# Optimization experiments

Measured on AMD Instinct MI355X. Metric: run time of the kernel, lower is better.

The kernel has to match this reference:

```python
import jax, jax.numpy as jnp
import numpy as np

D = 2048
NUM_HEADS = 16
HEAD_DIM = D // NUM_HEADS
B, T = 4, 2048
NEG = -1e9


def setup_inputs() -> dict:
    key = jax.random.key(0)
    ks = jax.random.split(key, 6)
    X = jax.random.normal(ks[0], (B, T, D), dtype=jnp.float32)
    # additive causal mask, broadcast over batch and heads
    causal = jnp.tril(jnp.ones((T, T), dtype=jnp.float32))
    mask = jnp.where(causal == 1, 0.0, NEG)[None, None, :, :]
    scale = np.sqrt(2.0 / D).astype(np.float32)
    wq_w = jax.random.normal(ks[1], (D, D), dtype=jnp.float32) * scale
    wk_w = jax.random.normal(ks[2], (D, D), dtype=jnp.float32) * scale
    wv_w = jax.random.normal(ks[3], (D, D), dtype=jnp.float32) * scale
    wo_w = jax.random.normal(ks[4], (D, D), dtype=jnp.float32) * scale
    zeros = jnp.zeros((D,), dtype=jnp.float32)
    return {
        "X": X, "mask": mask,
        "wq_w": wq_w, "wq_b": zeros,
        "wk_w": wk_w, "wk_b": zeros,
        "wv_w": wv_w, "wv_b": zeros,
        "wo_w": wo_w, "wo_b": zeros,
    }


def reference(X, mask, wq_w, wq_b, wk_w, wk_b, wv_w, wv_b, wo_w, wo_b):
    b, t, d = X.shape
    # project and split heads: [b, h, t, hd]
    def proj(w, bias):
        return (X @ w + bias).reshape(b, t, NUM_HEADS, HEAD_DIM).transpose(0, 2, 1, 3)
    Q = proj(wq_w, wq_b)
    K = proj(wk_w, wk_b)
    V = proj(wv_w, wv_b)
    scores = jnp.einsum("bhqd,bhkd->bhqk", Q, K) / np.sqrt(HEAD_DIM).astype(X.dtype)
    scores = scores + mask
    A = jax.nn.softmax(scores, axis=-1)
    ctx = jnp.einsum("bhqk,bhkd->bhqd", A, V)  # [b, h, t, hd]
    ctx = ctx.transpose(0, 2, 1, 3).reshape(b, t, d)
    return ctx @ wo_w + wo_b
```

## Files before the change

kernel.cpp:

```cpp
#include <hip/hip_runtime.h>
#include <stdint.h>

#define DMODEL 2048
#define NH 16
#define HD 128
#define BATCH 4
#define SEQ 2048
#define MTOT (BATCH * SEQ)
#define LOG2E 1.44269504088896340736f

typedef __bf16 bf16x8 __attribute__((ext_vector_type(8)));
typedef float floatx4 __attribute__((ext_vector_type(4)));

__device__ __forceinline__ uint16_t f2b(float f) {
    union { float f; uint32_t i; } v; v.f = f;
    uint32_t r = v.i + 0x7fffu + ((v.i >> 16) & 1u);
    return (uint16_t)(r >> 16);
}

__global__ __launch_bounds__(256) void cvt_bf16(const float* __restrict__ in,
                                                uint16_t* __restrict__ out, int n) {
    const int i = (blockIdx.x * 256 + threadIdx.x) * 8;
    if (i >= n) return;
    const float4 a = *(const float4*)(in + i);
    const float4 b = *(const float4*)(in + i + 4);
    uint16_t v[8] __attribute__((aligned(16))) = {
        f2b(a.x), f2b(a.y), f2b(a.z), f2b(a.w),
        f2b(b.x), f2b(b.y), f2b(b.z), f2b(b.w)};
    *(uint4*)(out + i) = *(const uint4*)v;
}

__global__ __launch_bounds__(256) void tr_wf(const float* __restrict__ in,
                                             uint16_t* __restrict__ out) {
    __shared__ float t[64 * 69];
    const int tid = threadIdx.x;
    const int r0 = blockIdx.y * 64, c0 = blockIdx.x * 64;
    const int rr = tid >> 2, c16 = (tid & 3) << 4;
#pragma unroll
    for (int j = 0; j < 4; j++)
        *(float4*)&t[rr * 69 + c16 + j * 4] =
            *(const float4*)(in + (size_t)(r0 + rr) * DMODEL + c0 + c16 + j * 4);
    __syncthreads();
    const int oc = tid >> 2, r16 = (tid & 3) << 4;
    uint16_t v[16] __attribute__((aligned(16)));
#pragma unroll
    for (int j = 0; j < 16; j++) v[j] = f2b(t[(r16 + j) * 69 + oc]);
    uint16_t* o = out + (size_t)(c0 + oc) * DMODEL + r0 + r16;
    *(uint4*)o = *(const uint4*)v;
    *(uint4*)(o + 8) = *(const uint4*)(v + 8);
}

__global__ __launch_bounds__(256, 2) void gemm(const uint16_t* __restrict__ A,
                                               const uint16_t* __restrict__ Bt,
                                               const float* __restrict__ bias,
                                               void* __restrict__ Cout,
                                               float scale, int out_f32) {
    __shared__ __attribute__((aligned(16))) uint16_t As[128 * 32];
    __shared__ __attribute__((aligned(16))) uint16_t Bs[128 * 32];
    const int tid = threadIdx.x, lane = tid & 63, w = tid >> 6;
    const int wr = w >> 1, wc = w & 1;
    const int col = lane & 15, quad = lane >> 4;
    const long m0 = (long)blockIdx.y * 128, n0 = (long)blockIdx.x * 128;

    floatx4 acc[4][4];
#pragma unroll
    for (int i = 0; i < 4; i++)
#pragma unroll
        for (int j = 0; j < 4; j++) acc[i][j] = (floatx4){0.f, 0.f, 0.f, 0.f};

    const int srow = tid >> 2, sc = (tid & 3) << 3;
    const uint16_t* Ag0 = A + (m0 + srow) * DMODEL + sc;
    const uint16_t* Bg0 = Bt + (n0 + srow) * DMODEL + sc;
    const long rstep = (long)64 * DMODEL;

    for (int kt = 0; kt < DMODEL; kt += 32) {
        const uint4 a0 = *(const uint4*)(Ag0 + kt);
        const uint4 a1 = *(const uint4*)(Ag0 + rstep + kt);
        const uint4 b0 = *(const uint4*)(Bg0 + kt);
        const uint4 b1 = *(const uint4*)(Bg0 + rstep + kt);
        *(uint4*)&As[tid * 8] = a0;
        *(uint4*)&As[2048 + tid * 8] = a1;
        *(uint4*)&Bs[tid * 8] = b0;
        *(uint4*)&Bs[2048 + tid * 8] = b1;
        __syncthreads();
        bf16x8 af[4], bfr[4];
#pragma unroll
        for (int i = 0; i < 4; i++)
            af[i] = *(const bf16x8*)&As[(wr * 64 + i * 16 + col) * 32 + quad * 8];
#pragma unroll
        for (int j = 0; j < 4; j++)
            bfr[j] = *(const bf16x8*)&Bs[(wc * 64 + j * 16 + col) * 32 + quad * 8];
#pragma unroll
        for (int i = 0; i < 4; i++)
#pragma unroll
            for (int j = 0; j < 4; j++)
                acc[i][j] = __builtin_amdgcn_mfma_f32_16x16x32_bf16(af[i], bfr[j],
                                                                    acc[i][j], 0, 0, 0);
        __syncthreads();
    }

    float bv[4];
#pragma unroll
    for (int j = 0; j < 4; j++) bv[j] = bias[n0 + wc * 64 + j * 16 + col];
#pragma unroll
    for (int i = 0; i < 4; i++) {
        const long row = m0 + wr * 64 + i * 16 + quad * 4;
#pragma unroll
        for (int j = 0; j < 4; j++) {
            const long cc = n0 + wc * 64 + j * 16 + col;
#pragma unroll
            for (int r = 0; r < 4; r++) {
                const float v = (acc[i][j][r] + bv[j]) * scale;
                const long idx = (row + r) * DMODEL + cc;
                if (out_f32) ((float*)Cout)[idx] = v;
                else         ((uint16_t*)Cout)[idx] = f2b(v);
            }
        }
    }
}

__global__ __launch_bounds__(256, 2) void flash(uint16_t* __restrict__ QO,
                                                const uint16_t* __restrict__ Kp,
                                                const uint16_t* __restrict__ Vp) {
    __shared__ __attribute__((aligned(16))) uint16_t Ks[4 * 64 * 32];
    __shared__ __attribute__((aligned(16))) uint16_t Vs[2 * 128 * 32];
    __shared__ __attribute__((aligned(16))) uint16_t Ps[4][32 * 88];

    const int tid = threadIdx.x, lane = tid & 63, w = tid >> 6;
    const int col = lane & 15, quad = lane >> 4;
    const int qi = blockIdx.x;
    const int h = blockIdx.y & 15, b = blockIdx.y >> 4;
    const int q0 = qi * 128;
    const size_t brow = (size_t)b * SEQ;

    uint16_t* qbase = QO + (brow + q0 + w * 32) * DMODEL + h * HD;

    bf16x8 qf[2][4];
#pragma unroll
    for (int i = 0; i < 2; i++)
#pragma unroll
        for (int kk = 0; kk < 4; kk++)
            qf[i][kk] = *(const bf16x8*)(qbase + (size_t)(i * 16 + col) * DMODEL +
                                         kk * 32 + quad * 8);

    floatx4 accO[2][8];
#pragma unroll
    for (int i = 0; i < 2; i++)
#pragma unroll
        for (int jd = 0; jd < 8; jd++) accO[i][jd] = (floatx4){0.f, 0.f, 0.f, 0.f};
    float mrun[2][4], lrun[2][4];
#pragma unroll
    for (int i = 0; i < 2; i++)
#pragma unroll
        for (int r = 0; r < 4; r++) { mrun[i][r] = -1e30f; lrun[i][r] = 0.f; }

    const uint16_t* kbase = Kp + brow * DMODEL + h * HD;
    const uint16_t* vbase = Vp + brow * DMODEL + h * HD;
    const int srow = tid >> 2;
    const int sc8 = (tid & 3) << 3;

    const int nkt = 2 * qi + 2;
    for (int ki = 0; ki < nkt; ki++) {
        const int key0 = ki * 64;
        {
            const uint16_t* kg = kbase + (size_t)(key0 + srow) * DMODEL + sc8;
            const uint16_t* vg = vbase + (size_t)(key0 + srow) * DMODEL + sc8;
            uint4 kv[4], vv4[4];
#pragma unroll
            for (int p = 0; p < 4; p++) {
                kv[p] = *(const uint4*)(kg + p * 32);
                vv4[p] = *(const uint4*)(vg + p * 32);
            }
#pragma unroll
            for (int p = 0; p < 4; p++)
                *(uint4*)&Ks[(p * 256 + tid) * 8] = kv[p];
            const int vb0 = ((srow >> 5) * 128) * 32 + (srow & 31);
#pragma unroll
            for (int p = 0; p < 4; p++) {
                uint16_t vals[8] __attribute__((aligned(16)));
                *(uint4*)vals = vv4[p];
                const int d0 = sc8 + p * 32;
#pragma unroll
                for (int j = 0; j < 8; j++) Vs[vb0 + (d0 + j) * 32] = vals[j];
            }
        }
        __syncthreads();

        floatx4 s[2][4];
#pragma unroll
        for (int i = 0; i < 2; i++)
#pragma unroll
            for (int jk = 0; jk < 4; jk++) {
                floatx4 a = (floatx4){0.f, 0.f, 0.f, 0.f};
#pragma unroll
                for (int kk = 0; kk < 4; kk++) {
                    bf16x8 bb = *(const bf16x8*)&Ks[(kk * 64 + jk * 16 + col) * 32 + quad * 8];
                    a = __builtin_amdgcn_mfma_f32_16x16x32_bf16(qf[i][kk], bb, a, 0, 0, 0);
                }
                s[i][jk] = a;
            }

        if (key0 + 63 > q0 + w * 32) {
#pragma unroll
            for (int i = 0; i < 2; i++) {
                const int qb = q0 + w * 32 + i * 16 + quad * 4;
#pragma unroll
                for (int jk = 0; jk < 4; jk++) {
                    const int key = key0 + jk * 16 + col;
#pragma unroll
                    for (int r = 0; r < 4; r++)
                        if (key > qb + r) s[i][jk][r] = -1e30f;
                }
            }
        }

        float alpha[2][4];
#pragma unroll
        for (int i = 0; i < 2; i++)
#pragma unroll
            for (int r = 0; r < 4; r++) {
                float mx = s[i][0][r];
#pragma unroll
                for (int jk = 1; jk < 4; jk++) mx = fmaxf(mx, s[i][jk][r]);
                mx = fmaxf(mx, __shfl_xor(mx, 1, 64));
                mx = fmaxf(mx, __shfl_xor(mx, 2, 64));
                mx = fmaxf(mx, __shfl_xor(mx, 4, 64));
                mx = fmaxf(mx, __shfl_xor(mx, 8, 64));
                mx = fmaxf(mx, mrun[i][r]);
                alpha[i][r] = exp2f((mrun[i][r] - mx) * LOG2E);
                mrun[i][r] = mx;
            }
#pragma unroll
        for (int i = 0; i < 2; i++)
#pragma unroll
            for (int r = 0; r < 4; r++) {
                float psum = 0.f;
#pragma unroll
                for (int jk = 0; jk < 4; jk++) {
                    const float p = exp2f((s[i][jk][r] - mrun[i][r]) * LOG2E);
                    psum += p;
                    Ps[w][(i * 16 + quad * 4 + r) * 88 + jk * 16 + col] = f2b(p);
                }
                lrun[i][r] = lrun[i][r] * alpha[i][r] + psum;
            }
#pragma unroll
        for (int i = 0; i < 2; i++)
#pragma unroll
            for (int jd = 0; jd < 8; jd++)
#pragma unroll
                for (int r = 0; r < 4; r++) accO[i][jd][r] *= alpha[i][r];

        bf16x8 pf[2][2];
#pragma unroll
        for (int i = 0; i < 2; i++)
#pragma unroll
            for (int k2 = 0; k2 < 2; k2++)
                pf[i][k2] = *(const bf16x8*)&Ps[w][(i * 16 + col) * 88 + k2 * 32 + quad * 8];
#pragma unroll
        for (int i = 0; i < 2; i++)
#pragma unroll
            for (int jd = 0; jd < 8; jd++)
#pragma unroll
                for (int k2 = 0; k2 < 2; k2++) {
                    bf16x8 vvv = *(const bf16x8*)&Vs[(k2 * 128 + jd * 16 + col) * 32 + quad * 8];
                    accO[i][jd] = __builtin_amdgcn_mfma_f32_16x16x32_bf16(pf[i][k2], vvv,
                                                                          accO[i][jd], 0, 0, 0);
                }
        __syncthreads();
    }

    float inv[2][4];
#pragma unroll
    for (int i = 0; i < 2; i++)
#pragma unroll
        for (int r = 0; r < 4; r++) {
            float l = lrun[i][r];
            l += __shfl_xor(l, 1, 64);
            l += __shfl_xor(l, 2, 64);
            l += __shfl_xor(l, 4, 64);
            l += __shfl_xor(l, 8, 64);
            inv[i][r] = 1.0f / l;
        }
#pragma unroll
    for (int i = 0; i < 2; i++)
#pragma unroll
        for (int jd = 0; jd < 8; jd++)
#pragma unroll
            for (int r = 0; r < 4; r++)
                qbase[(size_t)(i * 16 + quad * 4 + r) * DMODEL + jd * 16 + col] =
                    f2b(accO[i][jd][r] * inv[i][r]);
}

extern "C" void kernel_launch(void* const* d_in, const int* in_sizes, int n_in,
                              void* d_out, int out_size, void* d_ws, size_t ws_size,
                              hipStream_t stream) {
    const float* X   = (const float*)d_in[0];
    float*       msk = (float*)d_in[1];
    const float* wq  = (const float*)d_in[2];
    const float* wqb = (const float*)d_in[3];
    const float* wk  = (const float*)d_in[4];
    const float* wkb = (const float*)d_in[5];
    const float* wv  = (const float*)d_in[6];
    const float* wvb = (const float*)d_in[7];
    const float* wo  = (const float*)d_in[8];
    const float* wob = (const float*)d_in[9];
    float* out = (float*)d_out;

    char* ws = (char*)d_ws;
    const size_t MB = 1ull << 20;
    dim3 tb(256), gT(32, 32);
    const float qs = 0.08838834764831845f;

    if (ws_size >= 136 * MB) {
        uint16_t* Xb = (uint16_t*)(ws);
        uint16_t* Qb = (uint16_t*)(ws + 32 * MB);
        uint16_t* Kb = (uint16_t*)(ws + 64 * MB);
        uint16_t* Vb = (uint16_t*)(ws + 96 * MB);
        uint16_t* Wt = (uint16_t*)(ws + 128 * MB);
        dim3 gG(16, 64), gF(16, 64);
        cvt_bf16<<<8192, tb, 0, stream>>>(X, Xb, MTOT * DMODEL);
        tr_wf<<<gT, tb, 0, stream>>>(wq, Wt);
        gemm<<<gG, tb, 0, stream>>>(Xb, Wt, wqb, Qb, qs, 0);
        tr_wf<<<gT, tb, 0, stream>>>(wk, Wt);
        gemm<<<gG, tb, 0, stream>>>(Xb, Wt, wkb, Kb, 1.0f, 0);
        tr_wf<<<gT, tb, 0, stream>>>(wv, Wt);
        gemm<<<gG, tb, 0, stream>>>(Xb, Wt, wvb, Vb, 1.0f, 0);
        flash<<<gF, tb, 0, stream>>>(Qb, Kb, Vb);
        tr_wf<<<gT, tb, 0, stream>>>(wo, Wt);
        gemm<<<gG, tb, 0, stream>>>(Qb, Wt, wob, out, 1.0f, 1);
    } else {
        uint16_t* Xb = (uint16_t*)(ws);
        uint16_t* Qb = (uint16_t*)(ws + 8 * MB);
        uint16_t *Kb, *Vb, *Wt;
        if (ws_size >= 40 * MB) {
            Kb = (uint16_t*)(ws + 16 * MB);
            Vb = (uint16_t*)(ws + 24 * MB);
            Wt = (uint16_t*)(ws + 32 * MB);
        } else {
            Kb = (uint16_t*)msk;
            Vb = Kb + (size_t)SEQ * DMODEL;
            Wt = (uint16_t*)(ws + 16 * MB);
        }
        dim3 gG(16, 16), gF(16, 16);
        for (int b = 0; b < BATCH; b++) {
            const float* Xf = X + (size_t)b * SEQ * DMODEL;
            float* Ob = out + (size_t)b * SEQ * DMODEL;
            cvt_bf16<<<2048, tb, 0, stream>>>(Xf, Xb, SEQ * DMODEL);
            tr_wf<<<gT, tb, 0, stream>>>(wq, Wt);
            gemm<<<gG, tb, 0, stream>>>(Xb, Wt, wqb, Qb, qs, 0);
            tr_wf<<<gT, tb, 0, stream>>>(wk, Wt);
            gemm<<<gG, tb, 0, stream>>>(Xb, Wt, wkb, Kb, 1.0f, 0);
            tr_wf<<<gT, tb, 0, stream>>>(wv, Wt);
            gemm<<<gG, tb, 0, stream>>>(Xb, Wt, wvb, Vb, 1.0f, 0);
            flash<<<gF, tb, 0, stream>>>(Qb, Kb, Vb);
            tr_wf<<<gT, tb, 0, stream>>>(wo, Wt);
            gemm<<<gG, tb, 0, stream>>>(Qb, Wt, wob, Ob, 1.0f, 1);
        }
    }

    (void)in_sizes; (void)n_in; (void)out_size;
}
```

Measured before the change: 860.8 us.

## Pair causal query tiles per block, prefetch K/V, use direct global-to-LDS loads

The flash kernel now processes two query tiles per block, pairing tile 15-x with tile x, so every block does the same amount of causal work. The grid is halved to match. It also register-prefetches the next K/V tile while the current one is being computed. The GEMM staging swaps register-to-LDS copies for global_load_lds direct transfers, which depend on the per-wave LDS layout matching the old tid*8 ordering.

```diff
diff --git a/kernel.cpp b/kernel.cpp
--- a/kernel.cpp
+++ b/kernel.cpp
@@ -17,6 +17,11 @@
     uint32_t r = v.i + 0x7fffu + ((v.i >> 16) & 1u);
     return (uint16_t)(r >> 16);
 }
+
+#define GLD16(gp, lp)                                                          \
+    __builtin_amdgcn_global_load_lds(                                          \
+        (__attribute__((address_space(1))) unsigned int*)(gp),                 \
+        (__attribute__((address_space(3))) unsigned int*)(lp), 16, 0, 0)
 
 __global__ __launch_bounds__(256) void cvt_bf16(const float* __restrict__ in,
                                                 uint16_t* __restrict__ out, int n) {
@@ -72,16 +77,14 @@
     const uint16_t* Ag0 = A + (m0 + srow) * DMODEL + sc;
     const uint16_t* Bg0 = Bt + (n0 + srow) * DMODEL + sc;
     const long rstep = (long)64 * DMODEL;
+    uint16_t* AsW = &As[w * 512];
+    uint16_t* BsW = &Bs[w * 512];
 
     for (int kt = 0; kt < DMODEL; kt += 32) {
-        const uint4 a0 = *(const uint4*)(Ag0 + kt);
-        const uint4 a1 = *(const uint4*)(Ag0 + rstep + kt);
-        const uint4 b0 = *(const uint4*)(Bg0 + kt);
-        const uint4 b1 = *(const uint4*)(Bg0 + rstep + kt);
-        *(uint4*)&As[tid * 8] = a0;
-        *(uint4*)&As[2048 + tid * 8] = a1;
-        *(uint4*)&Bs[tid * 8] = b0;
-        *(uint4*)&Bs[2048 + tid * 8] = b1;
+        GLD16(Ag0 + kt, AsW);
+        GLD16(Ag0 + rstep + kt, AsW + 2048);
+        GLD16(Bg0 + kt, BsW);
+        GLD16(Bg0 + rstep + kt, BsW + 2048);
         __syncthreads();
         bf16x8 af[4], bfr[4];
 #pragma unroll
@@ -128,167 +131,183 @@
 
     const int tid = threadIdx.x, lane = tid & 63, w = tid >> 6;
     const int col = lane & 15, quad = lane >> 4;
-    const int qi = blockIdx.x;
     const int h = blockIdx.y & 15, b = blockIdx.y >> 4;
-    const int q0 = qi * 128;
     const size_t brow = (size_t)b * SEQ;
-
-    uint16_t* qbase = QO + (brow + q0 + w * 32) * DMODEL + h * HD;
-
-    bf16x8 qf[2][4];
-#pragma unroll
-    for (int i = 0; i < 2; i++)
-#pragma unroll
-        for (int kk = 0; kk < 4; kk++)
-            qf[i][kk] = *(const bf16x8*)(qbase + (size_t)(i * 16 + col) * DMODEL +
-                                         kk * 32 + quad * 8);
-
-    floatx4 accO[2][8];
-#pragma unroll
-    for (int i = 0; i < 2; i++)
-#pragma unroll
-        for (int jd = 0; jd < 8; jd++) accO[i][jd] = (floatx4){0.f, 0.f, 0.f, 0.f};
-    float mrun[2][4], lrun[2][4];
-#pragma unroll
-    for (int i = 0; i < 2; i++)
-#pragma unroll
-        for (int r = 0; r < 4; r++) { mrun[i][r] = -1e30f; lrun[i][r] = 0.f; }
 
     const uint16_t* kbase = Kp + brow * DMODEL + h * HD;
     const uint16_t* vbase = Vp + brow * DMODEL + h * HD;
     const int srow = tid >> 2;
     const int sc8 = (tid & 3) << 3;
 
-    const int nkt = 2 * qi + 2;
-    for (int ki = 0; ki < nkt; ki++) {
-        const int key0 = ki * 64;
+    for (int half = 0; half < 2; ++half) {
+        const int qi = half ? (int)blockIdx.x : (15 - (int)blockIdx.x);
+        const int q0 = qi * 128;
+        uint16_t* qbase = QO + (brow + q0 + w * 32) * DMODEL + h * HD;
+
+        bf16x8 qf[2][4];
+#pragma unroll
+        for (int i = 0; i < 2; i++)
+#pragma unroll
+            for (int kk = 0; kk < 4; kk++)
+                qf[i][kk] = *(const bf16x8*)(qbase + (size_t)(i * 16 + col) * DMODEL +
+                                             kk * 32 + quad * 8);
+
+        floatx4 accO[2][8];
+#pragma unroll
+        for (int i = 0; i < 2; i++)
+#pragma unroll
+            for (int jd = 0; jd < 8; jd++) accO[i][jd] = (floatx4){0.f, 0.f, 0.f, 0.f};
+        float mrun[2][4], lrun[2][4];
+#pragma unroll
+        for (int i = 0; i < 2; i++)
+#pragma unroll
+            for (int r = 0; r < 4; r++) { mrun[i][r] = -1e30f; lrun[i][r] = 0.f; }
+
+        const int nkt = 2 * qi + 2;
+
+        uint4 kv[4], vv4[4];
         {
-            const uint16_t* kg = kbase + (size_t)(key0 + srow) * DMODEL + sc8;
-            const uint16_t* vg = vbase + (size_t)(key0 + srow) * DMODEL + sc8;
-            uint4 kv[4], vv4[4];
+            const uint16_t* kg = kbase + (size_t)srow * DMODEL + sc8;
+            const uint16_t* vg = vbase + (size_t)srow * DMODEL + sc8;
 #pragma unroll
             for (int p = 0; p < 4; p++) {
                 kv[p] = *(const uint4*)(kg + p * 32);
                 vv4[p] = *(const uint4*)(vg + p * 32);
             }
+        }
+
+        for (int ki = 0; ki < nkt; ki++) {
+            const int key0 = ki * 64;
 #pragma unroll
             for (int p = 0; p < 4; p++)
                 *(uint4*)&Ks[(p * 256 + tid) * 8] = kv[p];
-            const int vb0 = ((srow >> 5) * 128) * 32 + (srow & 31);
-#pragma unroll
-            for (int p = 0; p < 4; p++) {
-                uint16_t vals[8] __attribute__((aligned(16)));
-                *(uint4*)vals = vv4[p];
-                const int d0 = sc8 + p * 32;
-#pragma unroll
-                for (int j = 0; j < 8; j++) Vs[vb0 + (d0 + j) * 32] = vals[j];
-            }
-        }
-        __syncthreads();
-
-        floatx4 s[2][4];
-#pragma unroll
-        for (int i = 0; i < 2; i++)
-#pragma unroll
-            for (int jk = 0; jk < 4; jk++) {
-                floatx4 a = (floatx4){0.f, 0.f, 0.f, 0.f};
-#pragma unroll
-                for (int kk = 0; kk < 4; kk++) {
-                    bf16x8 bb = *(const bf16x8*)&Ks[(kk * 64 + jk * 16 + col) * 32 + quad * 8];
-                    a = __builtin_amdgcn_mfma_f32_16x16x32_bf16(qf[i][kk], bb, a, 0, 0, 0);
-                }
-                s[i][jk] = a;
-            }
-
-        if (key0 + 63 > q0 + w * 32) {
-#pragma unroll
-            for (int i = 0; i < 2; i++) {
-                const int qb = q0 + w * 32 + i * 16 + quad * 4;
+            {
+                const int vb0 = ((srow >> 5) * 128) * 32 + (srow & 31);
+#pragma unroll
+                for (int p = 0; p < 4; p++) {
+                    uint16_t vals[8] __attribute__((aligned(16)));
+                    *(uint4*)vals = vv4[p];
+                    const int d0 = sc8 + p * 32;
+#pragma unroll
+                    for (int j = 0; j < 8; j++) Vs[vb0 + (d0 + j) * 32] = vals[j];
+                }
+            }
+            __syncthreads();
+
+            if (ki + 1 < nkt) {
+                const uint16_t* kg = kbase + (size_t)(key0 + 64 + srow) * DMODEL + sc8;
+                const uint16_t* vg = vbase + (size_t)(key0 + 64 + srow) * DMODEL + sc8;
+#pragma unroll
+                for (int p = 0; p < 4; p++) {
+                    kv[p] = *(const uint4*)(kg + p * 32);
+                    vv4[p] = *(const uint4*)(vg + p * 32);
+                }
+            }
+
+            floatx4 s[2][4];
+#pragma unroll
+            for (int i = 0; i < 2; i++)
 #pragma unroll
                 for (int jk = 0; jk < 4; jk++) {
-                    const int key = key0 + jk * 16 + col;
-#pragma unroll
-                    for (int r = 0; r < 4; r++)
-                        if (key > qb + r) s[i][jk][r] = -1e30f;
-                }
-            }
-        }
-
-        float alpha[2][4];
+                    floatx4 a = (floatx4){0.f, 0.f, 0.f, 0.f};
+#pragma unroll
+                    for (int kk = 0; kk < 4; kk++) {
+                        bf16x8 bb = *(const bf16x8*)&Ks[(kk * 64 + jk * 16 + col) * 32 + quad * 8];
+                        a = __builtin_amdgcn_mfma_f32_16x16x32_bf16(qf[i][kk], bb, a, 0, 0, 0);
+                    }
+                    s[i][jk] = a;
+                }
+
+            if (key0 + 63 > q0 + w * 32) {
+#pragma unroll
+                for (int i = 0; i < 2; i++) {
+                    const int qb = q0 + w * 32 + i * 16 + quad * 4;
+#pragma unroll
+                    for (int jk = 0; jk < 4; jk++) {
+                        const int key = key0 + jk * 16 + col;
+#pragma unroll
+                        for (int r = 0; r < 4; r++)
+                            if (key > qb + r) s[i][jk][r] = -1e30f;
+                    }
+                }
+            }
+
+            float alpha[2][4];
+#pragma unroll
+            for (int i = 0; i < 2; i++)
+#pragma unroll
+                for (int r = 0; r < 4; r++) {
+                    float mx = s[i][0][r];
+#pragma unroll
+                    for (int jk = 1; jk < 4; jk++) mx = fmaxf(mx, s[i][jk][r]);
+                    mx = fmaxf(mx, __shfl_xor(mx, 1, 64));
+                    mx = fmaxf(mx, __shfl_xor(mx, 2, 64));
+                    mx = fmaxf(mx, __shfl_xor(mx, 4, 64));
+                    mx = fmaxf(mx, __shfl_xor(mx, 8, 64));
+                    mx = fmaxf(mx, mrun[i][r]);
+                    alpha[i][r] = exp2f((mrun[i][r] - mx) * LOG2E);
+                    mrun[i][r] = mx;
+                }
+#pragma unroll
+            for (int i = 0; i < 2; i++)
+#pragma unroll
+                for (int r = 0; r < 4; r++) {
+                    float psum = 0.f;
+#pragma unroll
+                    for (int jk = 0; jk < 4; jk++) {
+                        const float p = exp2f((s[i][jk][r] - mrun[i][r]) * LOG2E);
+                        psum += p;
+                        Ps[w][(i * 16 + quad * 4 + r) * 88 + jk * 16 + col] = f2b(p);
+                    }
+                    lrun[i][r] = lrun[i][r] * alpha[i][r] + psum;
+                }
+#pragma unroll
+            for (int i = 0; i < 2; i++)
+#pragma unroll
+                for (int jd = 0; jd < 8; jd++)
+#pragma unroll
+                    for (int r = 0; r < 4; r++) accO[i][jd][r] *= alpha[i][r];
+
+            bf16x8 pf[2][2];
+#pragma unroll
+            for (int i = 0; i < 2; i++)
+#pragma unroll
+                for (int k2 = 0; k2 < 2; k2++)
+                    pf[i][k2] = *(const bf16x8*)&Ps[w][(i * 16 + col) * 88 + k2 * 32 + quad * 8];
+#pragma unroll
+            for (int i = 0; i < 2; i++)
+#pragma unroll
+                for (int jd = 0; jd < 8; jd++)
+#pragma unroll
+                    for (int k2 = 0; k2 < 2; k2++) {
+                        bf16x8 vvv = *(const bf16x8*)&Vs[(k2 * 128 + jd * 16 + col) * 32 + quad * 8];
+                        accO[i][jd] = __builtin_amdgcn_mfma_f32_16x16x32_bf16(pf[i][k2], vvv,
+                                                                              accO[i][jd], 0, 0, 0);
+                    }
+            __syncthreads();
+        }
+
+        float inv[2][4];
 #pragma unroll
         for (int i = 0; i < 2; i++)
 #pragma unroll
             for (int r = 0; r < 4; r++) {
-                float mx = s[i][0][r];
-#pragma unroll
-                for (int jk = 1; jk < 4; jk++) mx = fmaxf(mx, s[i][jk][r]);
-                mx = fmaxf(mx, __shfl_xor(mx, 1, 64));
-                mx = fmaxf(mx, __shfl_xor(mx, 2, 64));
-                mx = fmaxf(mx, __shfl_xor(mx, 4, 64));
-                mx = fmaxf(mx, __shfl_xor(mx, 8, 64));
-                mx = fmaxf(mx, mrun[i][r]);
-                alpha[i][r] = exp2f((mrun[i][r] - mx) * LOG2E);
-                mrun[i][r] = mx;
-            }
-#pragma unroll
-        for (int i = 0; i < 2; i++)
-#pragma unroll
-            for (int r = 0; r < 4; r++) {
-                float psum = 0.f;
-#pragma unroll
-                for (int jk = 0; jk < 4; jk++) {
-                    const float p = exp2f((s[i][jk][r] - mrun[i][r]) * LOG2E);
-                    psum += p;
-                    Ps[w][(i * 16 + quad * 4 + r) * 88 + jk * 16 + col] = f2b(p);
-                }
-                lrun[i][r] = lrun[i][r] * alpha[i][r] + psum;
+                float l = lrun[i][r];
+                l += __shfl_xor(l, 1, 64);
+                l += __shfl_xor(l, 2, 64);
+                l += __shfl_xor(l, 4, 64);
+                l += __shfl_xor(l, 8, 64);
+                inv[i][r] = 1.0f / l;
             }
 #pragma unroll
         for (int i = 0; i < 2; i++)
 #pragma unroll
             for (int jd = 0; jd < 8; jd++)
 #pragma unroll
-                for (int r = 0; r < 4; r++) accO[i][jd][r] *= alpha[i][r];
-
-        bf16x8 pf[2][2];
-#pragma unroll
-        for (int i = 0; i < 2; i++)
-#pragma unroll
-            for (int k2 = 0; k2 < 2; k2++)
-                pf[i][k2] = *(const bf16x8*)&Ps[w][(i * 16 + col) * 88 + k2 * 32 + quad * 8];
-#pragma unroll
-        for (int i = 0; i < 2; i++)
-#pragma unroll
-            for (int jd = 0; jd < 8; jd++)
-#pragma unroll
-                for (int k2 = 0; k2 < 2; k2++) {
-                    bf16x8 vvv = *(const bf16x8*)&Vs[(k2 * 128 + jd * 16 + col) * 32 + quad * 8];
-                    accO[i][jd] = __builtin_amdgcn_mfma_f32_16x16x32_bf16(pf[i][k2], vvv,
-                                                                          accO[i][jd], 0, 0, 0);
-                }
-        __syncthreads();
+                for (int r = 0; r < 4; r++)
+                    qbase[(size_t)(i * 16 + quad * 4 + r) * DMODEL + jd * 16 + col] =
+                        f2b(accO[i][jd][r] * inv[i][r]);
     }
-
-    float inv[2][4];
-#pragma unroll
-    for (int i = 0; i < 2; i++)
-#pragma unroll
-        for (int r = 0; r < 4; r++) {
-            float l = lrun[i][r];
-            l += __shfl_xor(l, 1, 64);
-            l += __shfl_xor(l, 2, 64);
-            l += __shfl_xor(l, 4, 64);
-            l += __shfl_xor(l, 8, 64);
-            inv[i][r] = 1.0f / l;
-        }
-#pragma unroll
-    for (int i = 0; i < 2; i++)
-#pragma unroll
-        for (int jd = 0; jd < 8; jd++)
-#pragma unroll
-            for (int r = 0; r < 4; r++)
-                qbase[(size_t)(i * 16 + quad * 4 + r) * DMODEL + jd * 16 + col] =
-                    f2b(accO[i][jd][r] * inv[i][r]);
 }
 
 extern "C" void kernel_launch(void* const* d_in, const int* in_sizes, int n_in,
@@ -317,7 +336,7 @@
         uint16_t* Kb = (uint16_t*)(ws + 64 * MB);
         uint16_t* Vb = (uint16_t*)(ws + 96 * MB);
         uint16_t* Wt = (uint16_t*)(ws + 128 * MB);
-        dim3 gG(16, 64), gF(16, 64);
+        dim3 gG(16, 64), gF(8, 64);
         cvt_bf16<<<8192, tb, 0, stream>>>(X, Xb, MTOT * DMODEL);
         tr_wf<<<gT, tb, 0, stream>>>(wq, Wt);
         gemm<<<gG, tb, 0, stream>>>(Xb, Wt, wqb, Qb, qs, 0);
@@ -341,7 +360,7 @@
             Vb = Kb + (size_t)SEQ * DMODEL;
             Wt = (uint16_t*)(ws + 16 * MB);
         }
-        dim3 gG(16, 16), gF(16, 16);
+        dim3 gG(16, 16), gF(8, 16);
         for (int b = 0; b < BATCH; b++) {
             const float* Xf = X + (size_t)b * SEQ * DMODEL;
             float* Ob = out + (size_t)b * SEQ * DMODEL;
```

After: 760.4 us. 11.7% less time.
